# Kernel tuning notes

Hardware: AMD Instinct MI355X
Metric: run time of the kernel (lower is better)

The kernel has to match this reference:

```python
import jax, jax.numpy as jnp
import numpy as np

D = 768
N_HEADS = 12
D_HEAD = D // N_HEADS


def setup_inputs() -> dict:
    key = jax.random.key(0)
    ks = jax.random.split(key, 7)
    B, S = 4, 2048
    sequence = jax.random.normal(ks[0], (B, S, D), dtype=jnp.float32)
    s = 1.0 / np.sqrt(D_HEAD)
    # Per-head Linear(d_head, d_head): weight [H, d_head, d_head] (torch layout: out,in), bias [H, d_head]
    Wq = jax.random.uniform(ks[1], (N_HEADS, D_HEAD, D_HEAD), minval=-s, maxval=s, dtype=jnp.float32)
    Wk = jax.random.uniform(ks[2], (N_HEADS, D_HEAD, D_HEAD), minval=-s, maxval=s, dtype=jnp.float32)
    Wv = jax.random.uniform(ks[3], (N_HEADS, D_HEAD, D_HEAD), minval=-s, maxval=s, dtype=jnp.float32)
    bq = jax.random.uniform(ks[4], (N_HEADS, D_HEAD), minval=-s, maxval=s, dtype=jnp.float32)
    bk = jax.random.uniform(ks[5], (N_HEADS, D_HEAD), minval=-s, maxval=s, dtype=jnp.float32)
    bv = jax.random.uniform(ks[6], (N_HEADS, D_HEAD), minval=-s, maxval=s, dtype=jnp.float32)
    return {"sequence": sequence, "Wq": Wq, "Wk": Wk, "Wv": Wv, "bq": bq, "bk": bk, "bv": bv}


def reference(sequence, Wq, Wk, Wv, bq, bk, bv):
    B, S, _ = sequence.shape
    # split channels into heads: [B, S, H, d_head]
    x = sequence.reshape(B, S, N_HEADS, D_HEAD)
    # torch Linear: y = x @ W.T + b, applied per head
    q = jnp.einsum("bshd,hed->bshe", x, Wq) + bq
    k = jnp.einsum("bshd,hed->bshe", x, Wk) + bk
    v = jnp.einsum("bshd,hed->bshe", x, Wv) + bv
    scale = 1.0 / jnp.sqrt(jnp.asarray(D_HEAD, dtype=sequence.dtype))
    scores = jnp.einsum("bshe,bthe->bhst", q, k) * scale  # [B, H, S, S]
    attn = jax.nn.softmax(scores, axis=-1)
    out = jnp.einsum("bhst,bthe->bshe", attn, v)  # [B, S, H, d_head]
    return out.reshape(B, S, N_HEADS * D_HEAD)
```

## Files before the change

### kernel.cpp

```cpp
#include <hip/hip_runtime.h>
#include <hip/hip_bf16.h>

#define S_LEN 2048
#define NHEAD 12
#define NBH 48
#define DMODEL 768
#define BR 128
#define BC 128

typedef __bf16 bf16x8 __attribute__((ext_vector_type(8)));
typedef float f32x4  __attribute__((ext_vector_type(4)));
typedef float f32x16 __attribute__((ext_vector_type(16)));

union B8U { uint4 u; bf16x8 b; };

__device__ __forceinline__ unsigned bf16rne(float f) {
  unsigned u = __float_as_uint(f);
  return (u + 0x7fffu + ((u >> 16) & 1u)) >> 16;
}

__global__ __launch_bounds__(256)
void w_cvt(const float* __restrict__ Wq, const float* __restrict__ Wk,
           const float* __restrict__ Wv, unsigned short* __restrict__ Wb) {
  int idx = blockIdx.x * 256 + threadIdx.x;
  int mat = idx / 12288;
  int off = idx - mat * 12288;
  const float* src = (mat == 0) ? Wq : (mat == 1) ? Wk : Wv;
  float4 v = ((const float4*)src)[off];
  ushort4 o;
  o.x = (unsigned short)bf16rne(v.x);
  o.y = (unsigned short)bf16rne(v.y);
  o.z = (unsigned short)bf16rne(v.z);
  o.w = (unsigned short)bf16rne(v.w);
  ((ushort4*)(Wb + (size_t)mat * 49152))[off] = o;
}

__global__ __launch_bounds__(256)
void qkv_proj(const float* __restrict__ seq,
              const unsigned short* __restrict__ Wb,
              const float* __restrict__ bq, const float* __restrict__ bk,
              const float* __restrict__ bv,
              unsigned short* __restrict__ Qp, unsigned short* __restrict__ Kp,
              unsigned short* __restrict__ VTp) {
  __shared__ __align__(16) unsigned short xs[128][72];

  const int tid  = threadIdx.x;
  const int lane = tid & 63;
  const int wave = tid >> 6;
  const int L    = lane >> 5;
  const int l31  = lane & 31;
  const int bh    = blockIdx.x % NBH;
  const int stile = blockIdx.x / NBH;
  const int b = bh / NHEAD, h = bh % NHEAD;
  const int s0 = stile * 128;

#pragma unroll
  for (int p = 0; p < 8; ++p) {
    int f = tid + p * 256;
    int row = f >> 4, c4 = f & 15;
    float4 x = *(const float4*)&seq[((size_t)(b * S_LEN + s0 + row)) * DMODEL + h * 64 + c4 * 4];
    uint2 d;
    d.x = bf16rne(x.x) | (bf16rne(x.y) << 16);
    d.y = bf16rne(x.z) | (bf16rne(x.w) << 16);
    *(uint2*)&xs[row][c4 * 4] = d;
  }
  __syncthreads();

  bf16x8 af[4];
#pragma unroll
  for (int ks = 0; ks < 4; ++ks)
    af[ks] = *(const bf16x8*)&xs[wave * 32 + l31][ks * 16 + L * 8];

  unsigned short (*Rt)[72] = (unsigned short(*)[72])(&xs[wave * 32][0]);
  unsigned short (*Vt)[36] = (unsigned short(*)[36])(&xs[wave * 32][0]);

  const float qs = 0.18033688011112042f;

#pragma unroll
  for (int mat = 0; mat < 2; ++mat) {
    const float* bp0 = (mat == 0) ? bq : bk;
    const float sc = (mat == 0) ? qs : 1.0f;
    const size_t wofs = (size_t)mat * 49152 + (size_t)h * 4096;
    f32x16 acc[2];
#pragma unroll
    for (int nt = 0; nt < 2; ++nt) {
      const int e = nt * 32 + l31;
      bf16x8 wf[4];
#pragma unroll
      for (int i = 0; i < 16; ++i) acc[nt][i] = 0.f;
#pragma unroll
      for (int ks = 0; ks < 4; ++ks)
        wf[ks] = *(const bf16x8*)&Wb[wofs + (size_t)e * 64 + ks * 16 + L * 8];
#pragma unroll
      for (int ks = 0; ks < 4; ++ks)
        acc[nt] = __builtin_amdgcn_mfma_f32_32x32x16_bf16(wf[ks], af[ks], acc[nt], 0, 0, 0);
    }
#pragma unroll
    for (int nt = 0; nt < 2; ++nt)
#pragma unroll
      for (int rq = 0; rq < 4; ++rq) {
        int e0 = nt * 32 + 8 * rq + 4 * L;
        const float* bp = bp0 + h * 64 + e0;
        ushort4 pv;
        pv.x = (unsigned short)bf16rne((acc[nt][4 * rq + 0] + bp[0]) * sc);
        pv.y = (unsigned short)bf16rne((acc[nt][4 * rq + 1] + bp[1]) * sc);
        pv.z = (unsigned short)bf16rne((acc[nt][4 * rq + 2] + bp[2]) * sc);
        pv.w = (unsigned short)bf16rne((acc[nt][4 * rq + 3] + bp[3]) * sc);
        *(ushort4*)&Rt[l31][e0] = pv;
      }
    unsigned short* P = (mat == 0) ? Qp : Kp;
#pragma unroll
    for (int p = 0; p < 4; ++p) {
      int f = lane + p * 64;
      int row = f >> 3, c = f & 7;
      uint4 d = *(const uint4*)&Rt[row][c * 8];
      *(uint4*)&P[((size_t)bh * S_LEN + s0 + wave * 32 + row) * 64 + c * 8] = d;
    }
  }

  {
    f32x16 vacc[2];
#pragma unroll
    for (int nt = 0; nt < 2; ++nt) {
      const int e = nt * 32 + l31;
      bf16x8 wf[4];
#pragma unroll
      for (int i = 0; i < 16; ++i) vacc[nt][i] = 0.f;
#pragma unroll
      for (int ks = 0; ks < 4; ++ks)
        wf[ks] = *(const bf16x8*)&Wb[2 * 49152 + (size_t)h * 4096 + (size_t)e * 64 + ks * 16 + L * 8];
#pragma unroll
      for (int ks = 0; ks < 4; ++ks)
        vacc[nt] = __builtin_amdgcn_mfma_f32_32x32x16_bf16(af[ks], wf[ks], vacc[nt], 0, 0, 0);
    }
#pragma unroll
    for (int nt = 0; nt < 2; ++nt) {
      const int e = nt * 32 + l31;
      float bias = bv[h * 64 + e];
#pragma unroll
      for (int rq = 0; rq < 4; ++rq) {
        ushort4 pv;
        pv.x = (unsigned short)bf16rne(vacc[nt][4 * rq + 0] + bias);
        pv.y = (unsigned short)bf16rne(vacc[nt][4 * rq + 1] + bias);
        pv.z = (unsigned short)bf16rne(vacc[nt][4 * rq + 2] + bias);
        pv.w = (unsigned short)bf16rne(vacc[nt][4 * rq + 3] + bias);
        *(ushort4*)&Vt[e][8 * rq + 4 * L] = pv;
      }
    }
#pragma unroll
    for (int p = 0; p < 4; ++p) {
      int f = lane + p * 64;
      int row = f >> 2, c = f & 3;
      uint4 d = *(const uint4*)&Vt[row][c * 8];
      *(uint4*)&VTp[((size_t)bh * 64 + row) * S_LEN + s0 + wave * 32 + c * 8] = d;
    }
  }
}

__global__ __launch_bounds__(512)
void flash_attn(const unsigned short* __restrict__ Qp,
                const unsigned short* __restrict__ Kp,
                const unsigned short* __restrict__ VTp,
                float* __restrict__ out) {
  __shared__ __align__(16) char smem[71680];
  unsigned short (*Ks)[128][72]  = (unsigned short(*)[128][72])smem;
  unsigned short (*Vs)[64][136]  = (unsigned short(*)[64][136])(smem + 36864);

  const int tid  = threadIdx.x;
  const int wave = tid >> 6;
  const int lane = tid & 63;
  const int L    = lane >> 5;
  const int l31  = lane & 31;
  const int qw   = wave & 3;
  const int kh   = wave >> 2;
  const int bh = blockIdx.x % NBH;
  const int qx = blockIdx.x / NBH;
  const int b = bh / NHEAD, h = bh % NHEAD;
  const int q0 = qx * BR;

  bf16x8 qfrag[4];
  {
    const uint4* Qv = (const uint4*)Qp;
#pragma unroll
    for (int ks = 0; ks < 4; ++ks) {
      B8U t;
      t.u = Qv[((size_t)bh * S_LEN + q0 + qw * 32 + l31) * 8 + ks * 2 + L];
      qfrag[ks] = t.b;
    }
  }

  f32x16 oacc[2];
#pragma unroll
  for (int mt = 0; mt < 2; ++mt)
#pragma unroll
    for (int i = 0; i < 16; ++i) oacc[mt][i] = 0.f;
  float l_run = 0.f;

  const uint4* Kv = (const uint4*)Kp  + (size_t)bh * S_LEN * 8;
  const uint4* Vv = (const uint4*)VTp + (size_t)bh * 64 * 256;

  uint4 kd[2], vd[2];
#pragma unroll
  for (int j = 0; j < 2; ++j) {
    int f = tid + j * 512;
    kd[j] = Kv[(size_t)(f >> 3) * 8 + (f & 7)];
    vd[j] = Vv[(size_t)(f >> 4) * 256 + (f & 15)];
  }

  int cur = 0;
  auto EPV = [&](const f32x16& sc, int tt) {
    unsigned pk[8];
    float la = 0.f, lb = 0.f;
#pragma unroll
    for (int p = 0; p < 8; ++p) {
      unsigned u0 = __float_as_uint(__builtin_amdgcn_exp2f(sc[2 * p]));
      unsigned u1 = __float_as_uint(__builtin_amdgcn_exp2f(sc[2 * p + 1]));
      unsigned d = __builtin_amdgcn_perm(u1, u0, 0x07060302);
      pk[p] = d;
      la += __uint_as_float(d << 16);
      lb += __uint_as_float(d & 0xffff0000u);
    }
    l_run += la + lb;
#pragma unroll
    for (int mk = 0; mk < 2; ++mk) {
      const int m = 2 * tt + mk;
      unsigned a0 = pk[4 * mk + 0], a1 = pk[4 * mk + 1];
      unsigned b0 = pk[4 * mk + 2], b1 = pk[4 * mk + 3];
      asm("v_permlane32_swap_b32 %0, %1" : "+v"(a0), "+v"(b0));
      asm("v_permlane32_swap_b32 %0, %1" : "+v"(a1), "+v"(b1));
      B8U t;
      t.u.x = a0; t.u.y = a1; t.u.z = b0; t.u.w = b1;
      __builtin_amdgcn_s_setprio(1);
#pragma unroll
      for (int mt = 0; mt < 2; ++mt) {
        bf16x8 va = *(const bf16x8*)&Vs[cur][mt * 32 + l31][m * 16 + L * 8];
        oacc[mt] = __builtin_amdgcn_mfma_f32_32x32x16_bf16(va, t.b, oacc[mt], 0, 0, 0);
      }
      __builtin_amdgcn_s_setprio(0);
    }
  };

#pragma unroll
  for (int j = 0; j < 2; ++j) {
    int f = tid + j * 512;
    *(uint4*)&Ks[0][f >> 3][(f & 7) * 8]  = kd[j];
    *(uint4*)&Vs[0][f >> 4][(f & 15) * 8] = vd[j];
  }
  __syncthreads();

  for (int i = 0; i < S_LEN / BC; ++i) {
    if (i + 1 < S_LEN / BC) {
      int t0n = (i + 1) * BC;
#pragma unroll
      for (int j = 0; j < 2; ++j) {
        int f = tid + j * 512;
        kd[j] = Kv[(size_t)(t0n + (f >> 3)) * 8 + (f & 7)];
        vd[j] = Vv[(size_t)(f >> 4) * 256 + (t0n >> 3) + (f & 15)];
      }
    }

    f32x16 sacc[2];
#pragma unroll
    for (int tl = 0; tl < 2; ++tl)
#pragma unroll
      for (int j = 0; j < 16; ++j) sacc[tl][j] = 0.f;

    __builtin_amdgcn_s_setprio(1);
#pragma unroll
    for (int ks = 0; ks < 4; ++ks)
#pragma unroll
      for (int tl = 0; tl < 2; ++tl) {
        bf16x8 a = *(const bf16x8*)&Ks[cur][(kh * 2 + tl) * 32 + l31][ks * 16 + L * 8];
        sacc[tl] = __builtin_amdgcn_mfma_f32_32x32x16_bf16(a, qfrag[ks], sacc[tl], 0, 0, 0);
      }
    __builtin_amdgcn_s_setprio(0);

    EPV(sacc[0], kh * 2 + 0);
    EPV(sacc[1], kh * 2 + 1);

    if (i + 1 < S_LEN / BC) {
#pragma unroll
      for (int j = 0; j < 2; ++j) {
        int f = tid + j * 512;
        *(uint4*)&Ks[cur ^ 1][f >> 3][(f & 7) * 8]  = kd[j];
        *(uint4*)&Vs[cur ^ 1][f >> 4][(f & 15) * 8] = vd[j];
      }
    }
    __syncthreads();
    cur ^= 1;
  }

  l_run += __shfl_xor(l_run, 32, 64);

  float* M  = (float*)smem;
  float* Ml = (float*)(smem + 34816);
  if (kh == 1) {
    float* Mw = M + qw * (32 * 68);
#pragma unroll
    for (int mt = 0; mt < 2; ++mt)
#pragma unroll
      for (int rq = 0; rq < 4; ++rq) {
        f32x4 v;
        v.x = oacc[mt][4 * rq + 0];
        v.y = oacc[mt][4 * rq + 1];
        v.z = oacc[mt][4 * rq + 2];
        v.w = oacc[mt][4 * rq + 3];
        int e0 = mt * 32 + 8 * rq + 4 * L;
        *(f32x4*)&Mw[l31 * 68 + e0] = v;
      }
    if (lane < 32) Ml[qw * 32 + l31] = l_run;
  }
  __syncthreads();
  if (kh == 0) {
    float* Mw = M + qw * (32 * 68);
#pragma unroll
    for (int mt = 0; mt < 2; ++mt)
#pragma unroll
      for (int rq = 0; rq < 4; ++rq) {
        int e0 = mt * 32 + 8 * rq + 4 * L;
        f32x4 v = *(const f32x4*)&Mw[l31 * 68 + e0];
        oacc[mt][4 * rq + 0] += v.x;
        oacc[mt][4 * rq + 1] += v.y;
        oacc[mt][4 * rq + 2] += v.z;
        oacc[mt][4 * rq + 3] += v.w;
      }
    l_run += Ml[qw * 32 + l31];
  }
  __syncthreads();

  if (kh == 0) {
    float* Os = (float*)smem + qw * (32 * 68);
    float inv = 1.0f / l_run;
#pragma unroll
    for (int mt = 0; mt < 2; ++mt)
#pragma unroll
      for (int rq = 0; rq < 4; ++rq) {
        f32x4 v;
        v.x = oacc[mt][4 * rq + 0] * inv;
        v.y = oacc[mt][4 * rq + 1] * inv;
        v.z = oacc[mt][4 * rq + 2] * inv;
        v.w = oacc[mt][4 * rq + 3] * inv;
        int e0 = mt * 32 + 8 * rq + 4 * L;
        *(f32x4*)&Os[l31 * 68 + e0] = v;
      }
#pragma unroll
    for (int p = 0; p < 8; ++p) {
      int q = (lane >> 4) + 4 * p;
      int e4 = lane & 15;
      float4 t = *(const float4*)&Os[q * 68 + e4 * 4];
      *(float4*)&out[((size_t)(b * S_LEN + q0 + qw * 32 + q)) * DMODEL + h * 64 + e4 * 4] = t;
    }
  }
}

extern "C" void kernel_launch(void* const* d_in, const int* in_sizes, int n_in,
                              void* d_out, int out_size, void* d_ws, size_t ws_size,
                              hipStream_t stream) {
  const float* seq = (const float*)d_in[0];
  const float* Wq  = (const float*)d_in[1];
  const float* Wk  = (const float*)d_in[2];
  const float* Wv  = (const float*)d_in[3];
  const float* bq  = (const float*)d_in[4];
  const float* bk  = (const float*)d_in[5];
  const float* bv  = (const float*)d_in[6];
  float* out = (float*)d_out;

  const size_t wb = 3 * 49152 * sizeof(unsigned short);
  const size_t qb = (size_t)NBH * S_LEN * 64 * sizeof(unsigned short);
  unsigned short* Wb  = (unsigned short*)d_ws;
  unsigned short* Qp  = (unsigned short*)((char*)d_ws + wb);
  unsigned short* Kp  = (unsigned short*)((char*)d_ws + wb + qb);
  unsigned short* VTp = (unsigned short*)((char*)d_ws + wb + 2 * qb);

  w_cvt<<<dim3(144), 256, 0, stream>>>(Wq, Wk, Wv, Wb);
  qkv_proj<<<dim3(16 * NBH), 256, 0, stream>>>(seq, Wb, bq, bk, bv, Qp, Kp, VTp);
  flash_attn<<<dim3(16 * NBH), 512, 0, stream>>>(Qp, Kp, VTp, out);
}
```

Baseline: 159.3 us.

## Halve attention KV tile, raise occupancy, fold weight conversion into projection

```diff
diff --git a/kernel.cpp b/kernel.cpp
--- a/kernel.cpp
+++ b/kernel.cpp
@@ -6,7 +6,8 @@
 #define NBH 48
 #define DMODEL 768
 #define BR 128
-#define BC 128
+#define BC 64
+#define NIT (S_LEN / BC)
 
 typedef __bf16 bf16x8 __attribute__((ext_vector_type(8)));
 typedef float f32x4  __attribute__((ext_vector_type(4)));
@@ -20,24 +21,9 @@
 }
 
 __global__ __launch_bounds__(256)
-void w_cvt(const float* __restrict__ Wq, const float* __restrict__ Wk,
-           const float* __restrict__ Wv, unsigned short* __restrict__ Wb) {
-  int idx = blockIdx.x * 256 + threadIdx.x;
-  int mat = idx / 12288;
-  int off = idx - mat * 12288;
-  const float* src = (mat == 0) ? Wq : (mat == 1) ? Wk : Wv;
-  float4 v = ((const float4*)src)[off];
-  ushort4 o;
-  o.x = (unsigned short)bf16rne(v.x);
-  o.y = (unsigned short)bf16rne(v.y);
-  o.z = (unsigned short)bf16rne(v.z);
-  o.w = (unsigned short)bf16rne(v.w);
-  ((ushort4*)(Wb + (size_t)mat * 49152))[off] = o;
-}
-
-__global__ __launch_bounds__(256)
 void qkv_proj(const float* __restrict__ seq,
-              const unsigned short* __restrict__ Wb,
+              const float* __restrict__ Wq, const float* __restrict__ Wk,
+              const float* __restrict__ Wv,
               const float* __restrict__ bq, const float* __restrict__ bk,
               const float* __restrict__ bv,
               unsigned short* __restrict__ Qp, unsigned short* __restrict__ Kp,
@@ -76,11 +62,22 @@
 
   const float qs = 0.18033688011112042f;
 
+  auto wfrag = [&](const float* Wm, int e, int ks) -> bf16x8 {
+    const float4* wp = (const float4*)&Wm[((size_t)(h * 64 + e)) * 64 + ks * 16 + L * 8];
+    float4 w0 = wp[0], w1 = wp[1];
+    B8U t;
+    t.u.x = bf16rne(w0.x) | (bf16rne(w0.y) << 16);
+    t.u.y = bf16rne(w0.z) | (bf16rne(w0.w) << 16);
+    t.u.z = bf16rne(w1.x) | (bf16rne(w1.y) << 16);
+    t.u.w = bf16rne(w1.z) | (bf16rne(w1.w) << 16);
+    return t.b;
+  };
+
 #pragma unroll
   for (int mat = 0; mat < 2; ++mat) {
+    const float* Wm  = (mat == 0) ? Wq : Wk;
     const float* bp0 = (mat == 0) ? bq : bk;
     const float sc = (mat == 0) ? qs : 1.0f;
-    const size_t wofs = (size_t)mat * 49152 + (size_t)h * 4096;
     f32x16 acc[2];
 #pragma unroll
     for (int nt = 0; nt < 2; ++nt) {
@@ -89,8 +86,7 @@
 #pragma unroll
       for (int i = 0; i < 16; ++i) acc[nt][i] = 0.f;
 #pragma unroll
-      for (int ks = 0; ks < 4; ++ks)
-        wf[ks] = *(const bf16x8*)&Wb[wofs + (size_t)e * 64 + ks * 16 + L * 8];
+      for (int ks = 0; ks < 4; ++ks) wf[ks] = wfrag(Wm, e, ks);
 #pragma unroll
       for (int ks = 0; ks < 4; ++ks)
         acc[nt] = __builtin_amdgcn_mfma_f32_32x32x16_bf16(wf[ks], af[ks], acc[nt], 0, 0, 0);
@@ -127,8 +123,7 @@
 #pragma unroll
       for (int i = 0; i < 16; ++i) vacc[nt][i] = 0.f;
 #pragma unroll
-      for (int ks = 0; ks < 4; ++ks)
-        wf[ks] = *(const bf16x8*)&Wb[2 * 49152 + (size_t)h * 4096 + (size_t)e * 64 + ks * 16 + L * 8];
+      for (int ks = 0; ks < 4; ++ks) wf[ks] = wfrag(Wv, e, ks);
 #pragma unroll
       for (int ks = 0; ks < 4; ++ks)
         vacc[nt] = __builtin_amdgcn_mfma_f32_32x32x16_bf16(af[ks], wf[ks], vacc[nt], 0, 0, 0);
@@ -157,14 +152,14 @@
   }
 }
 
-__global__ __launch_bounds__(512)
+__global__ __launch_bounds__(512, 6)
 void flash_attn(const unsigned short* __restrict__ Qp,
                 const unsigned short* __restrict__ Kp,
                 const unsigned short* __restrict__ VTp,
                 float* __restrict__ out) {
-  __shared__ __align__(16) char smem[71680];
-  unsigned short (*Ks)[128][72]  = (unsigned short(*)[128][72])smem;
-  unsigned short (*Vs)[64][136]  = (unsigned short(*)[64][136])(smem + 36864);
+  __shared__ __align__(16) char smem[36864];
+  unsigned short (*Ks)[64][72] = (unsigned short(*)[64][72])smem;
+  unsigned short (*Vs)[64][72] = (unsigned short(*)[64][72])(smem + 18432);
 
   const int tid  = threadIdx.x;
   const int wave = tid >> 6;
@@ -199,16 +194,13 @@
   const uint4* Kv = (const uint4*)Kp  + (size_t)bh * S_LEN * 8;
   const uint4* Vv = (const uint4*)VTp + (size_t)bh * 64 * 256;
 
-  uint4 kd[2], vd[2];
-#pragma unroll
-  for (int j = 0; j < 2; ++j) {
-    int f = tid + j * 512;
-    kd[j] = Kv[(size_t)(f >> 3) * 8 + (f & 7)];
-    vd[j] = Vv[(size_t)(f >> 4) * 256 + (f & 15)];
-  }
+  const int f0 = tid;
+  uint4 kd, vd;
+  kd = Kv[(size_t)(f0 >> 3) * 8 + (f0 & 7)];
+  vd = Vv[(size_t)(f0 >> 3) * 256 + (f0 & 7)];
 
   int cur = 0;
-  auto EPV = [&](const f32x16& sc, int tt) {
+  auto EPV = [&](const f32x16& sc, int t) {
     unsigned pk[8];
     float la = 0.f, lb = 0.f;
 #pragma unroll
@@ -223,68 +215,51 @@
     l_run += la + lb;
 #pragma unroll
     for (int mk = 0; mk < 2; ++mk) {
-      const int m = 2 * tt + mk;
+      const int m = 2 * t + mk;
       unsigned a0 = pk[4 * mk + 0], a1 = pk[4 * mk + 1];
       unsigned b0 = pk[4 * mk + 2], b1 = pk[4 * mk + 3];
       asm("v_permlane32_swap_b32 %0, %1" : "+v"(a0), "+v"(b0));
       asm("v_permlane32_swap_b32 %0, %1" : "+v"(a1), "+v"(b1));
-      B8U t;
-      t.u.x = a0; t.u.y = a1; t.u.z = b0; t.u.w = b1;
+      B8U t2;
+      t2.u.x = a0; t2.u.y = a1; t2.u.z = b0; t2.u.w = b1;
       __builtin_amdgcn_s_setprio(1);
 #pragma unroll
       for (int mt = 0; mt < 2; ++mt) {
         bf16x8 va = *(const bf16x8*)&Vs[cur][mt * 32 + l31][m * 16 + L * 8];
-        oacc[mt] = __builtin_amdgcn_mfma_f32_32x32x16_bf16(va, t.b, oacc[mt], 0, 0, 0);
+        oacc[mt] = __builtin_amdgcn_mfma_f32_32x32x16_bf16(va, t2.b, oacc[mt], 0, 0, 0);
       }
       __builtin_amdgcn_s_setprio(0);
     }
   };
 
-#pragma unroll
-  for (int j = 0; j < 2; ++j) {
-    int f = tid + j * 512;
-    *(uint4*)&Ks[0][f >> 3][(f & 7) * 8]  = kd[j];
-    *(uint4*)&Vs[0][f >> 4][(f & 15) * 8] = vd[j];
-  }
+  *(uint4*)&Ks[0][f0 >> 3][(f0 & 7) * 8] = kd;
+  *(uint4*)&Vs[0][f0 >> 3][(f0 & 7) * 8] = vd;
   __syncthreads();
 
-  for (int i = 0; i < S_LEN / BC; ++i) {
-    if (i + 1 < S_LEN / BC) {
+  for (int i = 0; i < NIT; ++i) {
+    if (i + 1 < NIT) {
       int t0n = (i + 1) * BC;
-#pragma unroll
-      for (int j = 0; j < 2; ++j) {
-        int f = tid + j * 512;
-        kd[j] = Kv[(size_t)(t0n + (f >> 3)) * 8 + (f & 7)];
-        vd[j] = Vv[(size_t)(f >> 4) * 256 + (t0n >> 3) + (f & 15)];
-      }
-    }
-
-    f32x16 sacc[2];
-#pragma unroll
-    for (int tl = 0; tl < 2; ++tl)
-#pragma unroll
-      for (int j = 0; j < 16; ++j) sacc[tl][j] = 0.f;
+      kd = Kv[(size_t)(t0n + (f0 >> 3)) * 8 + (f0 & 7)];
+      vd = Vv[(size_t)(f0 >> 3) * 256 + (t0n >> 3) + (f0 & 7)];
+    }
+
+    f32x16 sacc;
+#pragma unroll
+    for (int j = 0; j < 16; ++j) sacc[j] = 0.f;
 
     __builtin_amdgcn_s_setprio(1);
 #pragma unroll
-    for (int ks = 0; ks < 4; ++ks)
-#pragma unroll
-      for (int tl = 0; tl < 2; ++tl) {
-        bf16x8 a = *(const bf16x8*)&Ks[cur][(kh * 2 + tl) * 32 + l31][ks * 16 + L * 8];
-        sacc[tl] = __builtin_amdgcn_mfma_f32_32x32x16_bf16(a, qfrag[ks], sacc[tl], 0, 0, 0);
-      }
+    for (int ks = 0; ks < 4; ++ks) {
+      bf16x8 a = *(const bf16x8*)&Ks[cur][kh * 32 + l31][ks * 16 + L * 8];
+      sacc = __builtin_amdgcn_mfma_f32_32x32x16_bf16(a, qfrag[ks], sacc, 0, 0, 0);
+    }
     __builtin_amdgcn_s_setprio(0);
 
-    EPV(sacc[0], kh * 2 + 0);
-    EPV(sacc[1], kh * 2 + 1);
-
-    if (i + 1 < S_LEN / BC) {
-#pragma unroll
-      for (int j = 0; j < 2; ++j) {
-        int f = tid + j * 512;
-        *(uint4*)&Ks[cur ^ 1][f >> 3][(f & 7) * 8]  = kd[j];
-        *(uint4*)&Vs[cur ^ 1][f >> 4][(f & 15) * 8] = vd[j];
-      }
+    EPV(sacc, kh);
+
+    if (i + 1 < NIT) {
+      *(uint4*)&Ks[cur ^ 1][f0 >> 3][(f0 & 7) * 8] = kd;
+      *(uint4*)&Vs[cur ^ 1][f0 >> 3][(f0 & 7) * 8] = vd;
     }
     __syncthreads();
     cur ^= 1;
@@ -365,14 +340,11 @@
   const float* bv  = (const float*)d_in[6];
   float* out = (float*)d_out;
 
-  const size_t wb = 3 * 49152 * sizeof(unsigned short);
   const size_t qb = (size_t)NBH * S_LEN * 64 * sizeof(unsigned short);
-  unsigned short* Wb  = (unsigned short*)d_ws;
-  unsigned short* Qp  = (unsigned short*)((char*)d_ws + wb);
-  unsigned short* Kp  = (unsigned short*)((char*)d_ws + wb + qb);
-  unsigned short* VTp = (unsigned short*)((char*)d_ws + wb + 2 * qb);
-
-  w_cvt<<<dim3(144), 256, 0, stream>>>(Wq, Wk, Wv, Wb);
-  qkv_proj<<<dim3(16 * NBH), 256, 0, stream>>>(seq, Wb, bq, bk, bv, Qp, Kp, VTp);
+  unsigned short* Qp  = (unsigned short*)d_ws;
+  unsigned short* Kp  = (unsigned short*)((char*)d_ws + qb);
+  unsigned short* VTp = (unsigned short*)((char*)d_ws + 2 * qb);
+
+  qkv_proj<<<dim3(16 * NBH), 256, 0, stream>>>(seq, Wq, Wk, Wv, bq, bk, bv, Qp, Kp, VTp);
   flash_attn<<<dim3(16 * NBH), 512, 0, stream>>>(Qp, Kp, VTp, out);
 }
```

Result: slower. 203.7 us (+27.8%).
